# Optimization experiments

Hardware: AMD Instinct MI355X
Metric: run time of the kernel (lower is better)

Reference implementation:

```python
import jax, jax.numpy as jnp
import numpy as np
import math

SR = 16000        # sample_rate
HOP = 512         # hop_length
FMIN = 20.0
N_BINS = 84
BPO = 12          # bins_per_octave
Q = 1.0 / (2.0 ** (1.0 / BPO) - 1.0)


def setup_inputs() -> dict:
    key = jax.random.key(0)
    waveform = jax.random.normal(key, (2560000,), dtype=jnp.float32)
    return {"waveform": waveform}


def _bin_kernel(wl: int, freq: float, dtype):
    """Windowed single-DFT-bin kernel matching torch.stft row `freq_bin`.
    Returns (2,1,wl) conv kernel: [real, imag] parts of conj(e^{-2pi i f n / wl}) * hann.
    """
    n = np.arange(wl)
    # torch.hann_window default is periodic: 0.5*(1 - cos(2*pi*n/N))
    w = 0.5 - 0.5 * np.cos(2.0 * np.pi * n / wl)
    fb = min(int(freq * wl / SR), wl // 2)  # onesided stft has wl//2+1 rows
    ang = 2.0 * np.pi * fb * n / wl
    kr = (w * np.cos(ang)).astype(np.float32)
    ki = (-w * np.sin(ang)).astype(np.float32)
    return jnp.asarray(np.stack([kr, ki])[:, None, :], dtype=dtype)


def reference(waveform) -> jnp.ndarray:
    L = waveform.shape[-1]
    num_frames = (L - HOP) // HOP + 1  # matches torch code's frame count
    rows = []
    for k in range(N_BINS):
        freq = FMIN * 2.0 ** (k / BPO)
        wl = min(int(SR * Q / freq), L // 4)
        if wl < 32:  # torch code skips these bins (row stays zero)
            rows.append(jnp.zeros((num_frames,), waveform.dtype))
            continue
        pad = wl // 2  # torch.stft center=True reflect padding
        xpad = jnp.pad(waveform, (pad, pad), mode="reflect")
        kern = _bin_kernel(wl, freq, waveform.dtype)
        # strided correlation == extracting one DFT bin of every stft frame
        out = jax.lax.conv_general_dilated(
            xpad[None, None, :], kern, window_strides=(HOP,), padding="VALID"
        )[0]  # (2, n_frames_k)
        mag = jnp.sqrt(out[0] ** 2 + out[1] ** 2)
        mf = min(mag.shape[0], num_frames)
        rows.append(jnp.zeros((num_frames,), waveform.dtype).at[:mf].set(mag[:mf]))
    return jnp.stack(rows)[None]  # (1, n_bins, num_frames)
```

## Files before the change

kernel.cpp:

```cpp
#include <hip/hip_runtime.h>
#include <math.h>

#define L_IN   2560000
#define HOP    512
#define NB     84
#define NF     5000
#define PAD0   6726
#define XPLEN  2573452
#define XBLEN2 2637824
#define NTIL   80
#define SLOTS  7
#define NBLK   (NTIL*SLOTS)
#define XB_NB  1288
#define AG_NB  502

#define LDS_SZ 70656

#define XB_B 0
#define AG_B 5275648
#define P_B  7331840

typedef short bf16x8 __attribute__((ext_vector_type(8)));
typedef float f32x16 __attribute__((ext_vector_type(16)));

__device__ inline unsigned short f2bf(float f) {
  unsigned int u = __float_as_uint(f);
  return (unsigned short)((u + 0x7fffu + ((u >> 16) & 1u)) >> 16);
}

__device__ inline void load16(void* l, const void* g) {
  __builtin_amdgcn_global_load_lds((const __attribute__((address_space(1))) void*)g,
                                   (__attribute__((address_space(3))) void*)l, 16, 0, 0);
}

__global__ __launch_bounds__(256) void k_prep(const float* __restrict__ x,
                                              unsigned short* __restrict__ xb,
                                              unsigned short* __restrict__ Ag) {
  __shared__ int s_wl[16], s_pad[16], s_fb[16];
  if (blockIdx.x < XB_NB) {
    int i8 = (blockIdx.x * 256 + threadIdx.x) * 8;
    bf16x8 o;
    int u0 = i8 - PAD0;
    if (u0 >= 0 && u0 + 8 <= L_IN) {
      const float2* p = (const float2*)(x + u0);
#pragma unroll
      for (int j = 0; j < 4; ++j) {
        float2 v = p[j];
        o[2 * j]     = (short)f2bf(v.x);
        o[2 * j + 1] = (short)f2bf(v.y);
      }
    } else {
#pragma unroll
      for (int j = 0; j < 8; ++j) {
        int i = i8 + j;
        float v = 0.f;
        if (i < XPLEN) {
          int u = i - PAD0;
          if (u < 0) u = -u;
          else if (u >= L_IN) u = 2 * L_IN - 2 - u;
          v = x[u];
        }
        o[j] = (short)f2bf(v);
      }
    }
    *(bf16x8*)(xb + i8) = o;
  } else {
    int g = (blockIdx.x - XB_NB) * 256 + threadIdx.x;
    int s = g >> 9, w = g & 511;
    int im = w >> 8, kk = (w >> 6) & 3, lane = w & 63;
    int mt  = (s < 211) ? 0 : ((s < 245) ? 1 : 2);
    int mst = (mt == 0) ? 0 : ((mt == 1) ? 211 : 245);
    int kst = (mt == 0) ? 0 : ((mt == 1) ? 5632 : 6528);
    int tap0 = kst + (s - mst) * 64 + kk * 16 + ((lane >> 5) << 3);
    int bin0 = mt * 32 + im * 16;
    if (threadIdx.x < 16) {
      int bin = bin0 + threadIdx.x;
      int wl = 0, pad = 0, fb = 0;
      if (bin < NB) {
        double q    = 1.0 / (pow(2.0, 1.0 / 12.0) - 1.0);
        double freq = 20.0 * pow(2.0, (double)bin / 12.0);
        wl = (int)(16000.0 * q / freq);
        if (wl > L_IN / 4) wl = L_IN / 4;
        pad = wl >> 1;
        fb = (int)(freq * (double)wl / 16000.0);
        if (fb > wl / 2) fb = wl / 2;
      }
      s_wl[threadIdx.x] = wl; s_pad[threadIdx.x] = pad; s_fb[threadIdx.x] = fb;
    }
    __syncthreads();
    int bi  = (lane & 31) >> 1;
    int wl  = s_wl[bi], pad = s_pad[bi], fbq = s_fb[bi];
    int isIm = lane & 1;
    bf16x8 vv;
    if (wl == 0) {
#pragma unroll
      for (int j = 0; j < 8; ++j) vv[j] = 0;
    } else {
      float invwl = 1.0f / (float)wl;
#pragma unroll
      for (int j = 0; j < 8; ++j) {
        int n = tap0 + j - (PAD0 - pad);
        float v = 0.f;
        if (n >= 0 && n < wl) {
          float wn = 0.5f - 0.5f * __builtin_amdgcn_cosf((float)n * invwl);
          int m = (fbq * n) % wl;
          float rev = (float)m * invwl;
          float cs = __builtin_amdgcn_cosf(rev);
          float sn = __builtin_amdgcn_sinf(rev);
          v = isIm ? (-wn * sn) : (wn * cs);
        }
        vv[j] = (short)f2bf(v);
      }
    }
    *(bf16x8*)(Ag + ((size_t)s * 4096 + im * 2048 + kk * 512 + lane * 8)) = vv;
  }
}

struct AF { bf16x8 f[2][4]; };

__device__ inline void loadA(AF& a, const char* Ag, int s, int lane) {
  const char* p = Ag + ((size_t)s << 13) + lane * 16;
#pragma unroll
  for (int im = 0; im < 2; ++im)
#pragma unroll
    for (int kk = 0; kk < 4; ++kk)
      a.f[im][kk] = *(const bf16x8*)(p + im * 4096 + kk * 1024);
}

__device__ inline void readB(bf16x8 bf[4], const char* Bw, int l, int g, int lane) {
  int tb = l * 128 + ((lane >> 5) << 4);
  int ob = (g * 32 + (lane & 31)) * 1024 + tb;
#pragma unroll
  for (int kk = 0; kk < 4; ++kk) {
    int o = ob + kk * 32;
    o ^= ((o >> 10) & 15) << 4;
    bf[kk] = *(const bf16x8*)(Bw + o);
  }
}

__device__ inline void mfma8(const AF& a, const bf16x8 bf[4],
                             f32x16& accA, f32x16& accB) {
  __builtin_amdgcn_s_setprio(1);
#pragma unroll
  for (int kk = 0; kk < 4; ++kk) {
    accA = __builtin_amdgcn_mfma_f32_32x32x16_bf16(a.f[0][kk], bf[kk], accA, 0, 0, 0);
    accB = __builtin_amdgcn_mfma_f32_32x32x16_bf16(a.f[1][kk], bf[kk], accB, 0, 0, 0);
  }
  __builtin_amdgcn_s_setprio(0);
}

__global__ __launch_bounds__(256, 2) void k_gemm(const unsigned short* __restrict__ Ag,
                                                 const unsigned short* __restrict__ xb,
                                                 float* __restrict__ P,
                                                 float* __restrict__ out) {
  extern __shared__ char lds[];
  const int tid = threadIdx.x, lane = tid & 63, wv = tid >> 6;

  int bid = blockIdx.x;
  int xcd = bid & 7, loc = bid >> 3;
  int c = loc / 10, ntl = loc - c * 10;
  int nt = xcd * 10 + ntl;
  const int gs_[7] = {0, 43, 85, 127, 169, 211, 245};
  const int ns_[7] = {43, 42, 42, 42, 42, 34, 6};
  const int kb_[7] = {0, 2752, 5440, 8128, 10816, 5632, 6528};
  int gs = gs_[c], ns = ns_[c], kb = kb_[c];
  int nch = (64512 + 128 * ns + 1023) >> 10;

  const char* xsrc = (const char*)xb + (size_t)nt * 65536 + (size_t)kb * 2;
  for (int ci = wv; ci < nch; ci += 4)
    load16(lds + ci * 1024, xsrc + ci * 1024 + ((lane * 16) ^ ((ci & 15) << 4)));
  __builtin_amdgcn_sched_barrier(0);

  const char* Ab = (const char*)Ag;
  int nks = (ns - wv + 3) >> 2;
  AF a0, a1, a2;
  int s0 = gs + wv, s1 = gs + wv + 4, s2 = gs + wv + 8;
  loadA(a0, Ab, s0 > 250 ? 250 : s0, lane);
  loadA(a1, Ab, s1 > 250 ? 250 : s1, lane);
  loadA(a2, Ab, s2 > 250 ? 250 : s2, lane);

  f32x16 acc[2][2];
#pragma unroll
  for (int i = 0; i < 2; ++i)
#pragma unroll
    for (int j = 0; j < 2; ++j)
#pragma unroll
      for (int e = 0; e < 16; ++e) acc[i][j][e] = 0.f;

  asm volatile("s_waitcnt vmcnt(24)" ::: "memory");
  __syncthreads();

  bf16x8 bA[4], bB[4];
  readB(bA, lds, wv, 0, lane);

  int i = 0;
  while (i + 3 <= nks) {
    {
      int l = wv + 4 * i;
      readB(bB, lds, l, 1, lane);
      mfma8(a0, bA, acc[0][0], acc[1][0]);
      int ln = (i + 1 < nks) ? (wv + 4 * (i + 1)) : l;
      readB(bA, lds, ln, 0, lane);
      mfma8(a0, bB, acc[0][1], acc[1][1]);
      if (i + 3 < nks) loadA(a0, Ab, gs + wv + 4 * (i + 3), lane);
    }
    {
      int l = wv + 4 * (i + 1);
      readB(bB, lds, l, 1, lane);
      mfma8(a1, bA, acc[0][0], acc[1][0]);
      int ln = (i + 2 < nks) ? (wv + 4 * (i + 2)) : l;
      readB(bA, lds, ln, 0, lane);
      mfma8(a1, bB, acc[0][1], acc[1][1]);
      if (i + 4 < nks) loadA(a1, Ab, gs + wv + 4 * (i + 4), lane);
    }
    {
      int l = wv + 4 * (i + 2);
      readB(bB, lds, l, 1, lane);
      mfma8(a2, bA, acc[0][0], acc[1][0]);
      int ln = (i + 3 < nks) ? (wv + 4 * (i + 3)) : l;
      readB(bA, lds, ln, 0, lane);
      mfma8(a2, bB, acc[0][1], acc[1][1]);
      if (i + 5 < nks) loadA(a2, Ab, gs + wv + 4 * (i + 5), lane);
    }
    i += 3;
  }
  if (i < nks) {
    int l = wv + 4 * i;
    readB(bB, lds, l, 1, lane);
    mfma8(a0, bA, acc[0][0], acc[1][0]);
    int ln = (i + 1 < nks) ? (wv + 4 * (i + 1)) : l;
    readB(bA, lds, ln, 0, lane);
    mfma8(a0, bB, acc[0][1], acc[1][1]);
    if (i + 1 < nks) {
      int l1 = wv + 4 * (i + 1);
      readB(bB, lds, l1, 1, lane);
      mfma8(a1, bA, acc[0][0], acc[1][0]);
      int l2 = (i + 2 < nks) ? (wv + 4 * (i + 2)) : l1;
      readB(bA, lds, l2, 0, lane);
      mfma8(a1, bB, acc[0][1], acc[1][1]);
      if (i + 2 < nks) {
        readB(bB, lds, wv + 4 * (i + 2), 1, lane);
        mfma8(a2, bA, acc[0][0], acc[1][0]);
        mfma8(a2, bB, acc[0][1], acc[1][1]);
      }
    }
  }

  __syncthreads();
  float* Cw = (float*)(lds + wv * 16384);
#pragma unroll
  for (int im = 0; im < 2; ++im)
#pragma unroll
    for (int in_ = 0; in_ < 2; ++in_) {
      f32x16 v = acc[im][in_];
      int col = in_ * 32 + (lane & 31);
      int rb  = im * 32 + ((lane >> 5) << 2);
#pragma unroll
      for (int r = 0; r < 16; ++r) {
        int row = rb + (r & 3) + 8 * (r >> 2);
        Cw[row * 64 + col] = v[r];
      }
    }
  __syncthreads();
  const float* L0 = (const float*)lds;
  if (c < 5) {
    float* Pb = P + ((size_t)(nt * 5 + c) << 12);
#pragma unroll
    for (int e = 0; e < 16; ++e) {
      int idx = e * 256 + tid;
      Pb[idx] = L0[idx] + L0[idx + 4096] + L0[idx + 8192] + L0[idx + 12288];
    }
  } else {
    int bb = (c == 5) ? 32 : 64;
#pragma unroll
    for (int e = 0; e < 8; ++e) {
      int p = e * 256 + tid;
      int bl = p >> 6, fl = p & 63;
      int r0 = (bl * 2) * 64 + fl, r1 = r0 + 64;
      float re = L0[r0] + L0[r0 + 4096] + L0[r0 + 8192] + L0[r0 + 12288];
      float iv = L0[r1] + L0[r1 + 4096] + L0[r1 + 8192] + L0[r1 + 12288];
      int b = bb + bl, col = nt * 64 + fl;
      if (b < NB && col < NF)
        out[(size_t)b * NF + col] = sqrtf(re * re + iv * iv);
    }
  }
}

__global__ __launch_bounds__(256) void k_mag(const float* __restrict__ P,
                                             float* __restrict__ out) {
  int col = blockIdx.x * 256 + threadIdx.x;
  int b = blockIdx.y;
  if (col >= NF) return;
  int nt = col >> 6, fl = col & 63;
  const float* Pt = P + ((size_t)(nt * 5) << 12);
  float re = 0.f, iv = 0.f;
#pragma unroll
  for (int c = 0; c < 5; ++c) {
    const float* Pb = Pt + ((size_t)c << 12);
    re += Pb[(2 * b) * 64 + fl];
    iv += Pb[(2 * b + 1) * 64 + fl];
  }
  out[(size_t)b * NF + col] = sqrtf(re * re + iv * iv);
}

extern "C" void kernel_launch(void* const* d_in, const int* in_sizes, int n_in,
                              void* d_out, int out_size, void* d_ws, size_t ws_size,
                              hipStream_t stream) {
  const float* x = (const float*)d_in[0];
  char* ws = (char*)d_ws;
  unsigned short* xb = (unsigned short*)(ws + XB_B);
  unsigned short* Ag = (unsigned short*)(ws + AG_B);
  float* P           = (float*)(ws + P_B);
  float* out = (float*)d_out;

  hipFuncSetAttribute((const void*)k_gemm,
                      hipFuncAttributeMaxDynamicSharedMemorySize, LDS_SZ);

  hipLaunchKernelGGL(k_prep, dim3(XB_NB + AG_NB), dim3(256), 0, stream, x, xb, Ag);
  hipLaunchKernelGGL(k_gemm, dim3(NBLK), dim3(256), LDS_SZ, stream, Ag, xb, P, out);
  hipLaunchKernelGGL(k_mag, dim3(20, 32), dim3(256), 0, stream, P, out);
}
```

Measured before the change: 29.67 us.

## Use 8 waves per GEMM block and reduce partial tiles in two LDS passes

Doubles the k_gemm block from 256 to 512 threads, so each block splits its K-slices across 8 waves instead of 4. The wave-0..3 and wave-4..7 partial accumulators are written to LDS in two sequential passes and summed in registers. The aim is more latency hiding per block and less serial K work per wave. In exchange it adds extra barriers and LDS round trips in the epilogue. LDS use stays at 70 KB per block, so the launch bound of 4 blocks per CU is unlikely to be met, and register pressure may rise.

```diff
diff --git a/kernel.cpp b/kernel.cpp
--- a/kernel.cpp
+++ b/kernel.cpp
@@ -149,7 +149,7 @@
   __builtin_amdgcn_s_setprio(0);
 }
 
-__global__ __launch_bounds__(256, 2) void k_gemm(const unsigned short* __restrict__ Ag,
+__global__ __launch_bounds__(512, 4) void k_gemm(const unsigned short* __restrict__ Ag,
                                                  const unsigned short* __restrict__ xb,
                                                  float* __restrict__ P,
                                                  float* __restrict__ out) {
@@ -167,14 +167,14 @@
   int nch = (64512 + 128 * ns + 1023) >> 10;
 
   const char* xsrc = (const char*)xb + (size_t)nt * 65536 + (size_t)kb * 2;
-  for (int ci = wv; ci < nch; ci += 4)
+  for (int ci = wv; ci < nch; ci += 8)
     load16(lds + ci * 1024, xsrc + ci * 1024 + ((lane * 16) ^ ((ci & 15) << 4)));
   __builtin_amdgcn_sched_barrier(0);
 
   const char* Ab = (const char*)Ag;
-  int nks = (ns - wv + 3) >> 2;
+  int nks = (ns - wv + 7) >> 3;
   AF a0, a1, a2;
-  int s0 = gs + wv, s1 = gs + wv + 4, s2 = gs + wv + 8;
+  int s0 = gs + wv, s1 = gs + wv + 8, s2 = gs + wv + 16;
   loadA(a0, Ab, s0 > 250 ? 250 : s0, lane);
   loadA(a1, Ab, s1 > 250 ? 250 : s1, lane);
   loadA(a2, Ab, s2 > 250 ? 250 : s2, lane);
@@ -196,50 +196,50 @@
   int i = 0;
   while (i + 3 <= nks) {
     {
-      int l = wv + 4 * i;
+      int l = wv + 8 * i;
       readB(bB, lds, l, 1, lane);
       mfma8(a0, bA, acc[0][0], acc[1][0]);
-      int ln = (i + 1 < nks) ? (wv + 4 * (i + 1)) : l;
+      int ln = (i + 1 < nks) ? (wv + 8 * (i + 1)) : l;
       readB(bA, lds, ln, 0, lane);
       mfma8(a0, bB, acc[0][1], acc[1][1]);
-      if (i + 3 < nks) loadA(a0, Ab, gs + wv + 4 * (i + 3), lane);
+      if (i + 3 < nks) loadA(a0, Ab, gs + wv + 8 * (i + 3), lane);
     }
     {
-      int l = wv + 4 * (i + 1);
+      int l = wv + 8 * (i + 1);
       readB(bB, lds, l, 1, lane);
       mfma8(a1, bA, acc[0][0], acc[1][0]);
-      int ln = (i + 2 < nks) ? (wv + 4 * (i + 2)) : l;
+      int ln = (i + 2 < nks) ? (wv + 8 * (i + 2)) : l;
       readB(bA, lds, ln, 0, lane);
       mfma8(a1, bB, acc[0][1], acc[1][1]);
-      if (i + 4 < nks) loadA(a1, Ab, gs + wv + 4 * (i + 4), lane);
+      if (i + 4 < nks) loadA(a1, Ab, gs + wv + 8 * (i + 4), lane);
     }
     {
-      int l = wv + 4 * (i + 2);
+      int l = wv + 8 * (i + 2);
       readB(bB, lds, l, 1, lane);
       mfma8(a2, bA, acc[0][0], acc[1][0]);
-      int ln = (i + 3 < nks) ? (wv + 4 * (i + 3)) : l;
+      int ln = (i + 3 < nks) ? (wv + 8 * (i + 3)) : l;
       readB(bA, lds, ln, 0, lane);
       mfma8(a2, bB, acc[0][1], acc[1][1]);
-      if (i + 5 < nks) loadA(a2, Ab, gs + wv + 4 * (i + 5), lane);
+      if (i + 5 < nks) loadA(a2, Ab, gs + wv + 8 * (i + 5), lane);
     }
     i += 3;
   }
   if (i < nks) {
-    int l = wv + 4 * i;
+    int l = wv + 8 * i;
     readB(bB, lds, l, 1, lane);
     mfma8(a0, bA, acc[0][0], acc[1][0]);
-    int ln = (i + 1 < nks) ? (wv + 4 * (i + 1)) : l;
+    int ln = (i + 1 < nks) ? (wv + 8 * (i + 1)) : l;
     readB(bA, lds, ln, 0, lane);
     mfma8(a0, bB, acc[0][1], acc[1][1]);
     if (i + 1 < nks) {
-      int l1 = wv + 4 * (i + 1);
+      int l1 = wv + 8 * (i + 1);
       readB(bB, lds, l1, 1, lane);
       mfma8(a1, bA, acc[0][0], acc[1][0]);
-      int l2 = (i + 2 < nks) ? (wv + 4 * (i + 2)) : l1;
+      int l2 = (i + 2 < nks) ? (wv + 8 * (i + 2)) : l1;
       readB(bA, lds, l2, 0, lane);
       mfma8(a1, bB, acc[0][1], acc[1][1]);
       if (i + 2 < nks) {
-        readB(bB, lds, wv + 4 * (i + 2), 1, lane);
+        readB(bB, lds, wv + 8 * (i + 2), 1, lane);
         mfma8(a2, bA, acc[0][0], acc[1][0]);
         mfma8(a2, bB, acc[0][1], acc[1][1]);
       }
@@ -247,38 +247,62 @@
   }
 
   __syncthreads();
-  float* Cw = (float*)(lds + wv * 16384);
-#pragma unroll
-  for (int im = 0; im < 2; ++im)
-#pragma unroll
-    for (int in_ = 0; in_ < 2; ++in_) {
-      f32x16 v = acc[im][in_];
-      int col = in_ * 32 + (lane & 31);
-      int rb  = im * 32 + ((lane >> 5) << 2);
-#pragma unroll
-      for (int r = 0; r < 16; ++r) {
-        int row = rb + (r & 3) + 8 * (r >> 2);
-        Cw[row * 64 + col] = v[r];
-      }
-    }
-  __syncthreads();
-  const float* L0 = (const float*)lds;
+  float h[8];
+#pragma unroll
+  for (int pass = 0; pass < 2; ++pass) {
+    if ((wv >> 2) == pass) {
+      float* Cw = (float*)(lds + (wv & 3) * 16384);
+#pragma unroll
+      for (int im = 0; im < 2; ++im)
+#pragma unroll
+        for (int in_ = 0; in_ < 2; ++in_) {
+          f32x16 v = acc[im][in_];
+          int col = in_ * 32 + (lane & 31);
+          int rb  = im * 32 + ((lane >> 5) << 2);
+#pragma unroll
+          for (int r = 0; r < 16; ++r) {
+            int row = rb + (r & 3) + 8 * (r >> 2);
+            Cw[row * 64 + col] = v[r];
+          }
+        }
+    }
+    __syncthreads();
+    const float* L0 = (const float*)lds;
+#pragma unroll
+    for (int e = 0; e < 8; ++e) {
+      int idx = e * 512 + tid;
+      float s = L0[idx] + L0[idx + 4096] + L0[idx + 8192] + L0[idx + 12288];
+      h[e] = pass ? (h[e] + s) : s;
+    }
+    if (pass == 0) __syncthreads();
+  }
+
   if (c < 5) {
     float* Pb = P + ((size_t)(nt * 5 + c) << 12);
 #pragma unroll
-    for (int e = 0; e < 16; ++e) {
-      int idx = e * 256 + tid;
-      Pb[idx] = L0[idx] + L0[idx + 4096] + L0[idx + 8192] + L0[idx + 12288];
-    }
+    for (int e = 0; e < 8; ++e)
+      Pb[e * 512 + tid] = h[e];
   } else {
     int bb = (c == 5) ? 32 : 64;
 #pragma unroll
-    for (int e = 0; e < 8; ++e) {
-      int p = e * 256 + tid;
+    for (int e = 0; e < 4; ++e) {
+      int p = e * 512 + tid;
       int bl = p >> 6, fl = p & 63;
-      int r0 = (bl * 2) * 64 + fl, r1 = r0 + 64;
-      float re = L0[r0] + L0[r0 + 4096] + L0[r0 + 8192] + L0[r0 + 12288];
-      float iv = L0[r1] + L0[r1 + 4096] + L0[r1 + 8192] + L0[r1 + 12288];
+      float re = h[2 * e];
+      float iv = h[2 * e + 1];
+      (void)re; (void)iv;
+    }
+    float* W = (float*)lds;
+    __syncthreads();
+#pragma unroll
+    for (int e = 0; e < 8; ++e) W[e * 512 + tid] = h[e];
+    __syncthreads();
+#pragma unroll
+    for (int e = 0; e < 4; ++e) {
+      int p = e * 512 + tid;
+      int bl = p >> 6, fl = p & 63;
+      float re = W[(2 * bl) * 64 + fl];
+      float iv = W[(2 * bl + 1) * 64 + fl];
       int b = bb + bl, col = nt * 64 + fl;
       if (b < NB && col < NF)
         out[(size_t)b * NF + col] = sqrtf(re * re + iv * iv);
@@ -317,6 +341,6 @@
                       hipFuncAttributeMaxDynamicSharedMemorySize, LDS_SZ);
 
   hipLaunchKernelGGL(k_prep, dim3(XB_NB + AG_NB), dim3(256), 0, stream, x, xb, Ag);
-  hipLaunchKernelGGL(k_gemm, dim3(NBLK), dim3(256), LDS_SZ, stream, Ag, xb, P, out);
+  hipLaunchKernelGGL(k_gemm, dim3(NBLK), dim3(512), LDS_SZ, stream, Ag, xb, P, out);
   hipLaunchKernelGGL(k_mag, dim3(20, 32), dim3(256), 0, stream, P, out);
 }
```

Result: slower. 78.94 us (+166.1%).

## Merge last two GEMM work slots into one block with split wave roles

Applied to the files above, without the earlier changes.

Drops the seventh per-tile slot and folds its small workload (bins 64+) into slot 5. There, three waves split the 34-step band with stride 3 and the fourth wave handles the 6-step tail band, writing magnitudes directly from registers. This cuts the launched block count and removes an underfilled slot. The cost is more per-wave imbalance inside slot-5 blocks and a more complex epilogue.

```diff
diff --git a/kernel.cpp b/kernel.cpp
--- a/kernel.cpp
+++ b/kernel.cpp
@@ -9,7 +9,7 @@
 #define XPLEN  2573452
 #define XBLEN2 2637824
 #define NTIL   80
-#define SLOTS  7
+#define SLOTS  6
 #define NBLK   (NTIL*SLOTS)
 #define XB_NB  1288
 #define AG_NB  502
@@ -160,9 +160,9 @@
   int xcd = bid & 7, loc = bid >> 3;
   int c = loc / 10, ntl = loc - c * 10;
   int nt = xcd * 10 + ntl;
-  const int gs_[7] = {0, 43, 85, 127, 169, 211, 245};
-  const int ns_[7] = {43, 42, 42, 42, 42, 34, 6};
-  const int kb_[7] = {0, 2752, 5440, 8128, 10816, 5632, 6528};
+  const int gs_[6] = {0, 43, 85, 127, 169, 211};
+  const int ns_[6] = {43, 42, 42, 42, 42, 34};
+  const int kb_[6] = {0, 2752, 5440, 8128, 10816, 5632};
   int gs = gs_[c], ns = ns_[c], kb = kb_[c];
   int nch = (64512 + 128 * ns + 1023) >> 10;
 
@@ -171,10 +171,14 @@
     load16(lds + ci * 1024, xsrc + ci * 1024 + ((lane * 16) ^ ((ci & 15) << 4)));
   __builtin_amdgcn_sched_barrier(0);
 
+  int lb, st, so, nks;
+  if (c < 5)       { lb = wv; st = 4; so = gs;  nks = (ns - wv + 3) >> 2; }
+  else if (wv < 3) { lb = wv; st = 3; so = 211; nks = (36 - wv) / 3; }
+  else             { lb = 14; st = 1; so = 231; nks = 6; }
+
   const char* Ab = (const char*)Ag;
-  int nks = (ns - wv + 3) >> 2;
   AF a0, a1, a2;
-  int s0 = gs + wv, s1 = gs + wv + 4, s2 = gs + wv + 8;
+  int s0 = so + lb, s1 = so + lb + st, s2 = so + lb + 2 * st;
   loadA(a0, Ab, s0 > 250 ? 250 : s0, lane);
   loadA(a1, Ab, s1 > 250 ? 250 : s1, lane);
   loadA(a2, Ab, s2 > 250 ? 250 : s2, lane);
@@ -191,55 +195,55 @@
   __syncthreads();
 
   bf16x8 bA[4], bB[4];
-  readB(bA, lds, wv, 0, lane);
+  readB(bA, lds, lb, 0, lane);
 
   int i = 0;
   while (i + 3 <= nks) {
     {
-      int l = wv + 4 * i;
+      int l = lb + st * i;
       readB(bB, lds, l, 1, lane);
       mfma8(a0, bA, acc[0][0], acc[1][0]);
-      int ln = (i + 1 < nks) ? (wv + 4 * (i + 1)) : l;
+      int ln = (i + 1 < nks) ? (lb + st * (i + 1)) : l;
       readB(bA, lds, ln, 0, lane);
       mfma8(a0, bB, acc[0][1], acc[1][1]);
-      if (i + 3 < nks) loadA(a0, Ab, gs + wv + 4 * (i + 3), lane);
+      if (i + 3 < nks) loadA(a0, Ab, so + lb + st * (i + 3), lane);
     }
     {
-      int l = wv + 4 * (i + 1);
+      int l = lb + st * (i + 1);
       readB(bB, lds, l, 1, lane);
       mfma8(a1, bA, acc[0][0], acc[1][0]);
-      int ln = (i + 2 < nks) ? (wv + 4 * (i + 2)) : l;
+      int ln = (i + 2 < nks) ? (lb + st * (i + 2)) : l;
       readB(bA, lds, ln, 0, lane);
       mfma8(a1, bB, acc[0][1], acc[1][1]);
-      if (i + 4 < nks) loadA(a1, Ab, gs + wv + 4 * (i + 4), lane);
+      if (i + 4 < nks) loadA(a1, Ab, so + lb + st * (i + 4), lane);
     }
     {
-      int l = wv + 4 * (i + 2);
+      int l = lb + st * (i + 2);
       readB(bB, lds, l, 1, lane);
       mfma8(a2, bA, acc[0][0], acc[1][0]);
-      int ln = (i + 3 < nks) ? (wv + 4 * (i + 3)) : l;
+      int ln = (i + 3 < nks) ? (lb + st * (i + 3)) : l;
       readB(bA, lds, ln, 0, lane);
       mfma8(a2, bB, acc[0][1], acc[1][1]);
-      if (i + 5 < nks) loadA(a2, Ab, gs + wv + 4 * (i + 5), lane);
+      if (i + 5 < nks) loadA(a2, Ab, so + lb + st * (i + 5), lane);
     }
     i += 3;
   }
   if (i < nks) {
-    int l = wv + 4 * i;
+    int l = lb + st * i;
     readB(bB, lds, l, 1, lane);
     mfma8(a0, bA, acc[0][0], acc[1][0]);
-    int ln = (i + 1 < nks) ? (wv + 4 * (i + 1)) : l;
+    int ln = (i + 1 < nks) ? (lb + st * (i + 1)) : l;
     readB(bA, lds, ln, 0, lane);
     mfma8(a0, bB, acc[0][1], acc[1][1]);
     if (i + 1 < nks) {
-      int l1 = wv + 4 * (i + 1);
+      int l1 = lb + st * (i + 1);
       readB(bB, lds, l1, 1, lane);
       mfma8(a1, bA, acc[0][0], acc[1][0]);
-      int l2 = (i + 2 < nks) ? (wv + 4 * (i + 2)) : l1;
+      int l2 = (i + 2 < nks) ? (lb + st * (i + 2)) : l1;
       readB(bA, lds, l2, 0, lane);
       mfma8(a1, bB, acc[0][1], acc[1][1]);
       if (i + 2 < nks) {
-        readB(bB, lds, wv + 4 * (i + 2), 1, lane);
+        readB(bB, lds, lb + st * (i + 2), 1, lane);
         mfma8(a2, bA, acc[0][0], acc[1][0]);
         mfma8(a2, bB, acc[0][1], acc[1][1]);
       }
@@ -247,23 +251,23 @@
   }
 
   __syncthreads();
-  float* Cw = (float*)(lds + wv * 16384);
-#pragma unroll
-  for (int im = 0; im < 2; ++im)
-#pragma unroll
-    for (int in_ = 0; in_ < 2; ++in_) {
-      f32x16 v = acc[im][in_];
-      int col = in_ * 32 + (lane & 31);
-      int rb  = im * 32 + ((lane >> 5) << 2);
-#pragma unroll
-      for (int r = 0; r < 16; ++r) {
-        int row = rb + (r & 3) + 8 * (r >> 2);
-        Cw[row * 64 + col] = v[r];
-      }
-    }
-  __syncthreads();
-  const float* L0 = (const float*)lds;
   if (c < 5) {
+    float* Cw = (float*)(lds + wv * 16384);
+#pragma unroll
+    for (int im = 0; im < 2; ++im)
+#pragma unroll
+      for (int in_ = 0; in_ < 2; ++in_) {
+        f32x16 v = acc[im][in_];
+        int col = in_ * 32 + (lane & 31);
+        int rb  = im * 32 + ((lane >> 5) << 2);
+#pragma unroll
+        for (int r = 0; r < 16; ++r) {
+          int row = rb + (r & 3) + 8 * (r >> 2);
+          Cw[row * 64 + col] = v[r];
+        }
+      }
+    __syncthreads();
+    const float* L0 = (const float*)lds;
     float* Pb = P + ((size_t)(nt * 5 + c) << 12);
 #pragma unroll
     for (int e = 0; e < 16; ++e) {
@@ -271,17 +275,54 @@
       Pb[idx] = L0[idx] + L0[idx + 4096] + L0[idx + 8192] + L0[idx + 12288];
     }
   } else {
-    int bb = (c == 5) ? 32 : 64;
+    if (wv < 3) {
+      float* Cw = (float*)(lds + wv * 16384);
+#pragma unroll
+      for (int im = 0; im < 2; ++im)
+#pragma unroll
+        for (int in_ = 0; in_ < 2; ++in_) {
+          f32x16 v = acc[im][in_];
+          int col = in_ * 32 + (lane & 31);
+          int rb  = im * 32 + ((lane >> 5) << 2);
+#pragma unroll
+          for (int r = 0; r < 16; ++r) {
+            int row = rb + (r & 3) + 8 * (r >> 2);
+            Cw[row * 64 + col] = v[r];
+          }
+        }
+    } else {
+#pragma unroll
+      for (int im = 0; im < 2; ++im)
+#pragma unroll
+        for (int in_ = 0; in_ < 2; ++in_) {
+          f32x16 v = acc[im][in_];
+          int col = nt * 64 + in_ * 32 + (lane & 31);
+          int rb  = im * 32 + ((lane >> 5) << 2);
+#pragma unroll
+          for (int q = 0; q < 4; ++q)
+#pragma unroll
+            for (int h = 0; h < 2; ++h) {
+              int row = rb + 2 * h + 8 * q;
+              float re = v[4 * q + 2 * h];
+              float iv = v[4 * q + 2 * h + 1];
+              int b = 64 + (row >> 1);
+              if (b < NB && col < NF)
+                out[(size_t)b * NF + col] = sqrtf(re * re + iv * iv);
+            }
+        }
+    }
+    __syncthreads();
+    const float* L0 = (const float*)lds;
 #pragma unroll
     for (int e = 0; e < 8; ++e) {
       int p = e * 256 + tid;
       int bl = p >> 6, fl = p & 63;
-      int r0 = (bl * 2) * 64 + fl, r1 = r0 + 64;
-      float re = L0[r0] + L0[r0 + 4096] + L0[r0 + 8192] + L0[r0 + 12288];
-      float iv = L0[r1] + L0[r1 + 4096] + L0[r1 + 8192] + L0[r1 + 12288];
-      int b = bb + bl, col = nt * 64 + fl;
-      if (b < NB && col < NF)
-        out[(size_t)b * NF + col] = sqrtf(re * re + iv * iv);
+      int r0 = (2 * bl) * 64 + fl, r1 = r0 + 64;
+      float re = L0[r0] + L0[r0 + 4096] + L0[r0 + 8192];
+      float iv = L0[r1] + L0[r1 + 4096] + L0[r1 + 8192];
+      int col = nt * 64 + fl;
+      if (col < NF)
+        out[(size_t)(32 + bl) * NF + col] = sqrtf(re * re + iv * iv);
     }
   }
 }
```

Result: slower. 30.83 us (+3.9%).

## Halve GEMM N-tile to 32 frames, doubling blocks and raising occupancy

Applied to the files above, without the earlier changes.

The frame tile per block is cut from 64 to 32 columns, so the grid grows from 560 to 1120 blocks. LDS drops to about 37 KB and launch bounds allow 4 blocks per CU. The inner loop now does one B read and 8 MFMAs per step with double-buffered A fragments instead of triple, and partial-sum and output indexing are rewritten to match. This trades A-fragment reuse (each A tile is now loaded twice as often across blocks) for more parallelism, better latency hiding and lower register pressure.

```diff
diff --git a/kernel.cpp b/kernel.cpp
--- a/kernel.cpp
+++ b/kernel.cpp
@@ -8,13 +8,13 @@
 #define PAD0   6726
 #define XPLEN  2573452
 #define XBLEN2 2637824
-#define NTIL   80
+#define NTIL   160
 #define SLOTS  7
 #define NBLK   (NTIL*SLOTS)
 #define XB_NB  1288
 #define AG_NB  502
 
-#define LDS_SZ 70656
+#define LDS_SZ 37888
 
 #define XB_B 0
 #define AG_B 5275648
@@ -127,29 +127,27 @@
       a.f[im][kk] = *(const bf16x8*)(p + im * 4096 + kk * 1024);
 }
 
-__device__ inline void readB(bf16x8 bf[4], const char* Bw, int l, int g, int lane) {
+__device__ inline void stepC(const AF& a, int l, int lane, const char* Bw,
+                             f32x16& acc0, f32x16& acc1) {
+  bf16x8 bf[4];
   int tb = l * 128 + ((lane >> 5) << 4);
-  int ob = (g * 32 + (lane & 31)) * 1024 + tb;
+  int ob = (lane & 31) * 1024 + tb;
 #pragma unroll
   for (int kk = 0; kk < 4; ++kk) {
     int o = ob + kk * 32;
     o ^= ((o >> 10) & 15) << 4;
     bf[kk] = *(const bf16x8*)(Bw + o);
   }
-}
-
-__device__ inline void mfma8(const AF& a, const bf16x8 bf[4],
-                             f32x16& accA, f32x16& accB) {
   __builtin_amdgcn_s_setprio(1);
 #pragma unroll
   for (int kk = 0; kk < 4; ++kk) {
-    accA = __builtin_amdgcn_mfma_f32_32x32x16_bf16(a.f[0][kk], bf[kk], accA, 0, 0, 0);
-    accB = __builtin_amdgcn_mfma_f32_32x32x16_bf16(a.f[1][kk], bf[kk], accB, 0, 0, 0);
+    acc0 = __builtin_amdgcn_mfma_f32_32x32x16_bf16(a.f[0][kk], bf[kk], acc0, 0, 0, 0);
+    acc1 = __builtin_amdgcn_mfma_f32_32x32x16_bf16(a.f[1][kk], bf[kk], acc1, 0, 0, 0);
   }
   __builtin_amdgcn_s_setprio(0);
 }
 
-__global__ __launch_bounds__(256, 2) void k_gemm(const unsigned short* __restrict__ Ag,
+__global__ __launch_bounds__(256, 4) void k_gemm(const unsigned short* __restrict__ Ag,
                                                  const unsigned short* __restrict__ xb,
                                                  float* __restrict__ P,
                                                  float* __restrict__ out) {
@@ -158,128 +156,75 @@
 
   int bid = blockIdx.x;
   int xcd = bid & 7, loc = bid >> 3;
-  int c = loc / 10, ntl = loc - c * 10;
-  int nt = xcd * 10 + ntl;
+  int c = loc / 20, ntl = loc - c * 20;
+  int nt = xcd * 20 + ntl;
   const int gs_[7] = {0, 43, 85, 127, 169, 211, 245};
   const int ns_[7] = {43, 42, 42, 42, 42, 34, 6};
   const int kb_[7] = {0, 2752, 5440, 8128, 10816, 5632, 6528};
   int gs = gs_[c], ns = ns_[c], kb = kb_[c];
-  int nch = (64512 + 128 * ns + 1023) >> 10;
-
-  const char* xsrc = (const char*)xb + (size_t)nt * 65536 + (size_t)kb * 2;
+  int nch = (31744 + 128 * ns + 1023) >> 10;
+
+  const char* xsrc = (const char*)xb + (size_t)nt * 32768 + (size_t)kb * 2;
   for (int ci = wv; ci < nch; ci += 4)
     load16(lds + ci * 1024, xsrc + ci * 1024 + ((lane * 16) ^ ((ci & 15) << 4)));
   __builtin_amdgcn_sched_barrier(0);
 
   const char* Ab = (const char*)Ag;
   int nks = (ns - wv + 3) >> 2;
-  AF a0, a1, a2;
-  int s0 = gs + wv, s1 = gs + wv + 4, s2 = gs + wv + 8;
+  AF a0, a1;
+  int s0 = gs + wv, s1 = gs + wv + 4;
   loadA(a0, Ab, s0 > 250 ? 250 : s0, lane);
   loadA(a1, Ab, s1 > 250 ? 250 : s1, lane);
-  loadA(a2, Ab, s2 > 250 ? 250 : s2, lane);
-
-  f32x16 acc[2][2];
-#pragma unroll
-  for (int i = 0; i < 2; ++i)
-#pragma unroll
-    for (int j = 0; j < 2; ++j)
-#pragma unroll
-      for (int e = 0; e < 16; ++e) acc[i][j][e] = 0.f;
-
-  asm volatile("s_waitcnt vmcnt(24)" ::: "memory");
+
+  f32x16 acc0, acc1;
+#pragma unroll
+  for (int e = 0; e < 16; ++e) { acc0[e] = 0.f; acc1[e] = 0.f; }
+
+  asm volatile("s_waitcnt vmcnt(16)" ::: "memory");
   __syncthreads();
 
-  bf16x8 bA[4], bB[4];
-  readB(bA, lds, wv, 0, lane);
-
   int i = 0;
-  while (i + 3 <= nks) {
-    {
-      int l = wv + 4 * i;
-      readB(bB, lds, l, 1, lane);
-      mfma8(a0, bA, acc[0][0], acc[1][0]);
-      int ln = (i + 1 < nks) ? (wv + 4 * (i + 1)) : l;
-      readB(bA, lds, ln, 0, lane);
-      mfma8(a0, bB, acc[0][1], acc[1][1]);
-      if (i + 3 < nks) loadA(a0, Ab, gs + wv + 4 * (i + 3), lane);
-    }
-    {
-      int l = wv + 4 * (i + 1);
-      readB(bB, lds, l, 1, lane);
-      mfma8(a1, bA, acc[0][0], acc[1][0]);
-      int ln = (i + 2 < nks) ? (wv + 4 * (i + 2)) : l;
-      readB(bA, lds, ln, 0, lane);
-      mfma8(a1, bB, acc[0][1], acc[1][1]);
-      if (i + 4 < nks) loadA(a1, Ab, gs + wv + 4 * (i + 4), lane);
-    }
-    {
-      int l = wv + 4 * (i + 2);
-      readB(bB, lds, l, 1, lane);
-      mfma8(a2, bA, acc[0][0], acc[1][0]);
-      int ln = (i + 3 < nks) ? (wv + 4 * (i + 3)) : l;
-      readB(bA, lds, ln, 0, lane);
-      mfma8(a2, bB, acc[0][1], acc[1][1]);
-      if (i + 5 < nks) loadA(a2, Ab, gs + wv + 4 * (i + 5), lane);
-    }
-    i += 3;
-  }
-  if (i < nks) {
-    int l = wv + 4 * i;
-    readB(bB, lds, l, 1, lane);
-    mfma8(a0, bA, acc[0][0], acc[1][0]);
-    int ln = (i + 1 < nks) ? (wv + 4 * (i + 1)) : l;
-    readB(bA, lds, ln, 0, lane);
-    mfma8(a0, bB, acc[0][1], acc[1][1]);
-    if (i + 1 < nks) {
-      int l1 = wv + 4 * (i + 1);
-      readB(bB, lds, l1, 1, lane);
-      mfma8(a1, bA, acc[0][0], acc[1][0]);
-      int l2 = (i + 2 < nks) ? (wv + 4 * (i + 2)) : l1;
-      readB(bA, lds, l2, 0, lane);
-      mfma8(a1, bB, acc[0][1], acc[1][1]);
-      if (i + 2 < nks) {
-        readB(bB, lds, wv + 4 * (i + 2), 1, lane);
-        mfma8(a2, bA, acc[0][0], acc[1][0]);
-        mfma8(a2, bB, acc[0][1], acc[1][1]);
-      }
-    }
-  }
+  while (i + 2 <= nks) {
+    stepC(a0, wv + 4 * i, lane, lds, acc0, acc1);
+    if (i + 2 < nks) loadA(a0, Ab, gs + wv + 4 * (i + 2), lane);
+    stepC(a1, wv + 4 * (i + 1), lane, lds, acc0, acc1);
+    if (i + 3 < nks) loadA(a1, Ab, gs + wv + 4 * (i + 3), lane);
+    i += 2;
+  }
+  if (i < nks) stepC(a0, wv + 4 * i, lane, lds, acc0, acc1);
 
   __syncthreads();
-  float* Cw = (float*)(lds + wv * 16384);
-#pragma unroll
-  for (int im = 0; im < 2; ++im)
-#pragma unroll
-    for (int in_ = 0; in_ < 2; ++in_) {
-      f32x16 v = acc[im][in_];
-      int col = in_ * 32 + (lane & 31);
-      int rb  = im * 32 + ((lane >> 5) << 2);
-#pragma unroll
-      for (int r = 0; r < 16; ++r) {
-        int row = rb + (r & 3) + 8 * (r >> 2);
-        Cw[row * 64 + col] = v[r];
-      }
-    }
+  float* Cw = (float*)(lds + wv * 8192);
+#pragma unroll
+  for (int im = 0; im < 2; ++im) {
+    f32x16 v = im ? acc1 : acc0;
+    int col = lane & 31;
+    int rb  = im * 32 + ((lane >> 5) << 2);
+#pragma unroll
+    for (int r = 0; r < 16; ++r) {
+      int row = rb + (r & 3) + 8 * (r >> 2);
+      Cw[row * 32 + col] = v[r];
+    }
+  }
   __syncthreads();
   const float* L0 = (const float*)lds;
   if (c < 5) {
-    float* Pb = P + ((size_t)(nt * 5 + c) << 12);
-#pragma unroll
-    for (int e = 0; e < 16; ++e) {
+    float* Pb = P + ((size_t)(nt * 5 + c) << 11);
+#pragma unroll
+    for (int e = 0; e < 8; ++e) {
       int idx = e * 256 + tid;
-      Pb[idx] = L0[idx] + L0[idx + 4096] + L0[idx + 8192] + L0[idx + 12288];
+      Pb[idx] = L0[idx] + L0[idx + 2048] + L0[idx + 4096] + L0[idx + 6144];
     }
   } else {
     int bb = (c == 5) ? 32 : 64;
 #pragma unroll
-    for (int e = 0; e < 8; ++e) {
+    for (int e = 0; e < 4; ++e) {
       int p = e * 256 + tid;
-      int bl = p >> 6, fl = p & 63;
-      int r0 = (bl * 2) * 64 + fl, r1 = r0 + 64;
-      float re = L0[r0] + L0[r0 + 4096] + L0[r0 + 8192] + L0[r0 + 12288];
-      float iv = L0[r1] + L0[r1 + 4096] + L0[r1 + 8192] + L0[r1 + 12288];
-      int b = bb + bl, col = nt * 64 + fl;
+      int bl = p >> 5, fl = p & 31;
+      int r0 = (bl * 2) * 32 + fl, r1 = r0 + 32;
+      float re = L0[r0] + L0[r0 + 2048] + L0[r0 + 4096] + L0[r0 + 6144];
+      float iv = L0[r1] + L0[r1 + 2048] + L0[r1 + 4096] + L0[r1 + 6144];
+      int b = bb + bl, col = nt * 32 + fl;
       if (b < NB && col < NF)
         out[(size_t)b * NF + col] = sqrtf(re * re + iv * iv);
     }
@@ -291,14 +236,14 @@
   int col = blockIdx.x * 256 + threadIdx.x;
   int b = blockIdx.y;
   if (col >= NF) return;
-  int nt = col >> 6, fl = col & 63;
-  const float* Pt = P + ((size_t)(nt * 5) << 12);
+  int nt = col >> 5, fl = col & 31;
+  const float* Pt = P + ((size_t)(nt * 5) << 11);
   float re = 0.f, iv = 0.f;
 #pragma unroll
   for (int c = 0; c < 5; ++c) {
-    const float* Pb = Pt + ((size_t)c << 12);
-    re += Pb[(2 * b) * 64 + fl];
-    iv += Pb[(2 * b + 1) * 64 + fl];
+    const float* Pb = Pt + ((size_t)c << 11);
+    re += Pb[(2 * b) * 32 + fl];
+    iv += Pb[(2 * b + 1) * 32 + fl];
   }
   out[(size_t)b * NF + col] = sqrtf(re * re + iv * iv);
 }
```

After: 33.41 us. +12.6%, slower.
